# Optimization experiments

Hardware: AMD Instinct MI355X
Metric: run time of the kernel (lower is better)

## Reference

```python
import jax, jax.numpy as jnp
import numpy as np

GROUPS = 8
EPS = 1e-3  # keras GroupNormalization default epsilon


def group_norm(x, gamma, beta):
    # x: [B,H,W,C], groups over channel axis
    B, H, W, C = x.shape
    g = GROUPS
    xr = x.reshape(B, H, W, g, C // g)
    mean = jnp.mean(xr, axis=(1, 2, 4), keepdims=True)
    var = jnp.var(xr, axis=(1, 2, 4), keepdims=True)
    xn = (xr - mean) * jax.lax.rsqrt(var + EPS)
    xn = xn.reshape(B, H, W, C)
    return xn * gamma + beta


def setup_inputs() -> dict:
    key = jax.random.key(0)
    ks = jax.random.split(key, 6)
    B, H, W, C = 8, 64, 64, 64
    std = 0.02
    return {
        "x": jax.random.normal(ks[0], (B, H, W, C), dtype=jnp.float32),
        "gamma": jnp.ones((C,), dtype=jnp.float32),
        "beta": jnp.zeros((C,), dtype=jnp.float32),
        "wq": jax.random.normal(ks[1], (C, C), dtype=jnp.float32) * std,
        "bq": jnp.zeros((C,), dtype=jnp.float32),
        "wk": jax.random.normal(ks[2], (C, C), dtype=jnp.float32) * std,
        "bk": jnp.zeros((C,), dtype=jnp.float32),
        "wv": jax.random.normal(ks[3], (C, C), dtype=jnp.float32) * std,
        "bv": jnp.zeros((C,), dtype=jnp.float32),
        "wp": jax.random.normal(ks[4], (C, C), dtype=jnp.float32) * std,
        "bp": jnp.zeros((C,), dtype=jnp.float32),
    }


def reference(x, gamma, beta, wq, bq, wk, bk, wv, bv, wp, bp):
    B, H, W, C = x.shape
    scale = jnp.asarray(C, x.dtype) ** -0.5
    h = group_norm(x, gamma, beta)  # note: residual uses normalized input (as in source)
    q = h @ wq + bq
    k = h @ wk + bk
    v = h @ wv + bv
    # full O((HW)^2) score tensor, exactly as the original
    attn = jnp.einsum('bhwc,bHWc->bhwHW', q, k) * scale
    attn = jax.nn.softmax(attn.reshape(B, H, W, H * W), axis=-1)
    attn = attn.reshape(B, H, W, H, W)
    proj = jnp.einsum('bhwHW,bHWc->bhwc', attn, v)
    proj = proj @ wp + bp
    return h + proj
```

## Files before the change

### kernel.cpp

```cpp
#include <hip/hip_runtime.h>

#define NTOK 4096
#define CH 64
#define LOG2E 1.4426950408889634f

typedef __bf16 bf8 __attribute__((ext_vector_type(8)));
typedef __bf16 bf4 __attribute__((ext_vector_type(4)));
typedef _Float16 h8 __attribute__((ext_vector_type(8)));
typedef _Float16 h4 __attribute__((ext_vector_type(4)));
typedef float f4 __attribute__((ext_vector_type(4)));

__device__ __forceinline__ f4 mfma16(bf8 a, bf8 b, f4 c) {
    return __builtin_amdgcn_mfma_f32_16x16x32_bf16(a, b, c, 0, 0, 0);
}
__device__ __forceinline__ f4 mfma16h(h4 a, h4 b, f4 c) {
    return __builtin_amdgcn_mfma_f32_16x16x16f16(a, b, c, 0, 0, 0);
}

__global__ __launch_bounds__(256) void pre_kernel(const float* __restrict__ wq,
                                                  const float* __restrict__ wk,
                                                  const float* __restrict__ wv,
                                                  const float* __restrict__ wp,
                                                  const float* __restrict__ x,
                                                  __bf16* __restrict__ wqt,
                                                  __bf16* __restrict__ wkt,
                                                  __bf16* __restrict__ wvt,
                                                  __bf16* __restrict__ wpt,
                                                  float* __restrict__ gpart) {
    int t = threadIdx.x;
    if (blockIdx.x < 4) {
        int m = blockIdx.x;
        const float* src = (m == 0) ? wq : (m == 1) ? wk : (m == 2) ? wv : wp;
        __bf16* dst      = (m == 0) ? wqt : (m == 1) ? wkt : (m == 2) ? wvt : wpt;
        __shared__ float s[64][65];
        for (int i = 0; i < 16; ++i) {
            int e = i * 256 + t;
            s[e >> 6][e & 63] = src[e];
        }
        __syncthreads();
        int out = t >> 2, seg = t & 3;
        for (int j = 0; j < 16; ++j) {
            int in = seg * 16 + j;
            dst[out * 64 + in] = (__bf16)s[in][out];
        }
        return;
    }
    int bid = blockIdx.x - 4;
    int b = bid >> 6, slab = bid & 63;
    const float4* xb = (const float4*)(x + (size_t)(b * NTOK + slab * 64) * CH);
    float s = 0.f, ss = 0.f;
    for (int i = 0; i < 4; ++i) {
        int row = (t >> 4) + i * 16;
        float4 v = xb[row * 16 + (t & 15)];
        s  += v.x + v.y + v.z + v.w;
        ss += v.x * v.x + v.y * v.y + v.z * v.z + v.w * v.w;
    }
    __shared__ float ls[256], lss[256];
    ls[t] = s; lss[t] = ss;
    __syncthreads();
    if (t < 8) {
        float a = 0.f, aa = 0.f;
        for (int p = 0; p < 16; ++p) {
            a  += ls[p * 16 + 2 * t]  + ls[p * 16 + 2 * t + 1];
            aa += lss[p * 16 + 2 * t] + lss[p * 16 + 2 * t + 1];
        }
        gpart[((b * 64 + slab) * 8 + t) * 2 + 0] = a;
        gpart[((b * 64 + slab) * 8 + t) * 2 + 1] = aa;
    }
}

__global__ __launch_bounds__(256) void qkv_gn(const float* __restrict__ x,
                                              const float* __restrict__ gpart,
                                              const float* __restrict__ gamma,
                                              const float* __restrict__ beta,
                                              const __bf16* __restrict__ wqt,
                                              const __bf16* __restrict__ wkt,
                                              const __bf16* __restrict__ wvt,
                                              const float* __restrict__ bq,
                                              const float* __restrict__ bk,
                                              const float* __restrict__ bv,
                                              __bf16* __restrict__ q,
                                              __bf16* __restrict__ k,
                                              _Float16* __restrict__ vT) {
    __shared__ __bf16 W[3][64][72];
    __shared__ __bf16 Hl[64][72];
    __shared__ _Float16 Vst[64][68];
    __shared__ float red[128];
    __shared__ float sstat[16];
    int t = threadIdx.x;
    size_t rowbase = (size_t)blockIdx.x * 64;
    int b = (int)(rowbase >> 12), tokbase = (int)(rowbase & 4095);
    if (t < 64) {
        int gi = t & 7, c = t >> 3;
        const float2* gp = (const float2*)gpart + (size_t)b * 64 * 8 + gi;
        float a = 0.f, aa = 0.f;
        for (int p = c * 8; p < c * 8 + 8; ++p) {
            float2 v = gp[(size_t)p * 8];
            a += v.x; aa += v.y;
        }
        red[t * 2] = a; red[t * 2 + 1] = aa;
    }
    for (int m = 0; m < 3; ++m) {
        const __bf16* src = (m == 0) ? wqt : (m == 1) ? wkt : wvt;
        for (int i = 0; i < 2; ++i) {
            int e = i * 256 + t, row = e >> 3, ch = e & 7;
            *(bf8*)&W[m][row][ch * 8] = *(const bf8*)(src + row * 64 + ch * 8);
        }
    }
    __syncthreads();
    if (t < 8) {
        float a = 0.f, aa = 0.f;
        for (int c = 0; c < 8; ++c) {
            a  += red[(c * 8 + t) * 2];
            aa += red[(c * 8 + t) * 2 + 1];
        }
        float mean = a * (1.f / 32768.f);
        float var = aa * (1.f / 32768.f) - mean * mean;
        sstat[t * 2 + 0] = mean;
        sstat[t * 2 + 1] = rsqrtf(var + 1e-3f);
    }
    __syncthreads();
    {
        int c4 = (t & 15) * 4, grp = c4 >> 3;
        float mean = sstat[grp * 2], rstd = sstat[grp * 2 + 1];
        float g0 = gamma[c4] * rstd, g1 = gamma[c4 + 1] * rstd,
              g2 = gamma[c4 + 2] * rstd, g3 = gamma[c4 + 3] * rstd;
        float b0 = beta[c4], b1 = beta[c4 + 1], b2 = beta[c4 + 2], b3 = beta[c4 + 3];
        const float4* xb = (const float4*)(x + rowbase * 64);
        for (int i = 0; i < 4; ++i) {
            int row = (t >> 4) + i * 16;
            float4 v = xb[row * 16 + (t & 15)];
            bf4 hv;
            hv[0] = (__bf16)((v.x - mean) * g0 + b0);
            hv[1] = (__bf16)((v.y - mean) * g1 + b1);
            hv[2] = (__bf16)((v.z - mean) * g2 + b2);
            hv[3] = (__bf16)((v.w - mean) * g3 + b3);
            *(bf4*)&Hl[row][c4] = hv;
        }
    }
    __syncthreads();
    int lane = t & 63, wave = t >> 6, quad = lane >> 4, l15 = lane & 15;
    bf8 a0 = *(const bf8*)&Hl[wave * 16 + l15][quad * 8];
    bf8 a1 = *(const bf8*)&Hl[wave * 16 + l15][32 + quad * 8];
    for (int m = 0; m < 3; ++m) {
        const float* bias = (m == 0) ? bq : (m == 1) ? bk : bv;
        float sc = (m == 0) ? 0.125f * LOG2E : 1.0f;
        for (int tt = 0; tt < 4; ++tt) {
            int col = l15 + 16 * tt;
            bf8 b0 = *(const bf8*)&W[m][col][quad * 8];
            bf8 b1 = *(const bf8*)&W[m][col][32 + quad * 8];
            f4 acc = {0.f, 0.f, 0.f, 0.f};
            acc = mfma16(a0, b0, acc);
            acc = mfma16(a1, b1, acc);
            float bb = bias[col];
            if (m == 2) {
                for (int r = 0; r < 4; ++r)
                    Vst[col][wave * 16 + quad * 4 + r] = (_Float16)(acc[r] + bb);
            } else {
                __bf16* dst = (m == 0) ? q : k;
                for (int r = 0; r < 4; ++r) {
                    float val = (acc[r] + bb) * sc;
                    dst[(rowbase + wave * 16 + quad * 4 + r) * 64 + col] = (__bf16)val;
                }
            }
        }
    }
    __syncthreads();
    {
        int d = t >> 2, seg = t & 3;
        h4 c0 = *(const h4*)&Vst[d][seg * 16 + 0];
        h4 c1 = *(const h4*)&Vst[d][seg * 16 + 4];
        h4 c2 = *(const h4*)&Vst[d][seg * 16 + 8];
        h4 c3 = *(const h4*)&Vst[d][seg * 16 + 12];
        h8 o0 = {c0[0], c0[1], c0[2], c0[3], c1[0], c1[1], c1[2], c1[3]};
        h8 o1 = {c2[0], c2[1], c2[2], c2[3], c3[0], c3[1], c3[2], c3[3]};
        _Float16* dst = vT + (((size_t)b * 256 + (tokbase >> 4) + seg) * 64 + d) * 16;
        *(h8*)dst = o0;
        *(h8*)(dst + 8) = o1;
    }
}

__global__ __launch_bounds__(256, 2) void attn_final(const __bf16* __restrict__ q,
                                                     const __bf16* __restrict__ k,
                                                     const _Float16* __restrict__ vt,
                                                     const __bf16* __restrict__ wpt,
                                                     const float* __restrict__ bp,
                                                     const float* __restrict__ x,
                                                     const float* __restrict__ gpart,
                                                     const float* __restrict__ gamma,
                                                     const float* __restrict__ beta,
                                                     float* __restrict__ out) {
    __shared__ _Float16 Om[2][64][72];
    __shared__ float sS[2][64];
    __shared__ __bf16 Wl[64][72];
    __shared__ __bf16 Ol[64][72];
    __shared__ float red[128];
    __shared__ float sstat[16], sg[64], sb[64];

    int bid = blockIdx.x;
    int qt = bid >> 3, b = bid & 7;
    int t = threadIdx.x, lane = t & 63, w = t >> 6, quad = lane >> 4, l15 = lane & 15;

    for (int i = 0; i < 2; ++i) {
        int e = i * 256 + t, row = e >> 3, ch = e & 7;
        *(bf8*)&Wl[row][ch * 8] = *(const bf8*)(wpt + row * 64 + ch * 8);
    }
    if (t < 64) { sg[t] = gamma[t]; sb[t] = beta[t]; }
    if (t < 64) {
        int gi = t & 7, c = t >> 3;
        const float2* gp = (const float2*)gpart + (size_t)b * 512 + gi;
        float a = 0.f, aa = 0.f;
        for (int p = c * 8; p < c * 8 + 8; ++p) {
            float2 v = gp[(size_t)p * 8];
            a += v.x; aa += v.y;
        }
        red[t * 2] = a; red[t * 2 + 1] = aa;
    }

    const __bf16* qbase = q + ((size_t)b * NTOK + qt * 64) * 64;
    bf8 aq[4][2];
    for (int s = 0; s < 4; ++s) {
        const __bf16* r = qbase + (s * 16 + l15) * 64;
        aq[s][0] = *(const bf8*)(r + quad * 8);
        aq[s][1] = *(const bf8*)(r + 32 + quad * 8);
    }
    const __bf16* kr = k + ((size_t)b * NTOK + w * 1024 + l15) * 64;
    const _Float16* vr = vt + (size_t)b * 262144 + ((size_t)(w * 64) * 64 + l15) * 16 + quad * 4;

    f4 acc[4][4] = {};
    float li[4] = {0.f, 0.f, 0.f, 0.f};

    bf8 kf0 = *(const bf8*)(kr + quad * 8);
    bf8 kf1 = *(const bf8*)(kr + 32 + quad * 8);
    h4 vf0 = *(const h4*)(vr);
    h4 vf1 = *(const h4*)(vr + 256);
    h4 vf2 = *(const h4*)(vr + 512);
    h4 vf3 = *(const h4*)(vr + 768);

    #pragma unroll 1
    for (int it = 0; it < 64; ++it) {
        int nx = (it + 1) & 63;
        const __bf16* krn = kr + (size_t)nx * 1024;
        const _Float16* vrn = vr + (size_t)nx * 1024;
        bf8 nk0 = *(const bf8*)(krn + quad * 8);
        bf8 nk1 = *(const bf8*)(krn + 32 + quad * 8);
        h4 nv0 = *(const h4*)(vrn);
        h4 nv1 = *(const h4*)(vrn + 256);
        h4 nv2 = *(const h4*)(vrn + 512);
        h4 nv3 = *(const h4*)(vrn + 768);

        for (int s = 0; s < 4; ++s) {
            f4 St = {0.f, 0.f, 0.f, 0.f};
            St = mfma16(kf0, aq[s][0], St);
            St = mfma16(kf1, aq[s][1], St);
            h4 pf;
            for (int r = 0; r < 4; ++r) {
                float pv = __builtin_amdgcn_exp2f(St[r]);
                li[s] += pv;
                pf[r] = (_Float16)pv;
            }
            acc[s][0] = mfma16h(vf0, pf, acc[s][0]);
            acc[s][1] = mfma16h(vf1, pf, acc[s][1]);
            acc[s][2] = mfma16h(vf2, pf, acc[s][2]);
            acc[s][3] = mfma16h(vf3, pf, acc[s][3]);
        }
        kf0 = nk0; kf1 = nk1;
        vf0 = nv0; vf1 = nv1; vf2 = nv2; vf3 = nv3;
    }

    for (int s = 0; s < 4; ++s) {
        li[s] += __shfl_xor(li[s], 16);
        li[s] += __shfl_xor(li[s], 32);
    }

    if (w >= 2) {
        for (int s = 0; s < 4; ++s) {
            for (int td = 0; td < 4; ++td) {
                h4 o4;
                for (int r = 0; r < 4; ++r) o4[r] = (_Float16)acc[s][td][r];
                *(h4*)&Om[w - 2][s * 16 + l15][td * 16 + quad * 4] = o4;
            }
            if (quad == 0) sS[w - 2][s * 16 + l15] = li[s];
        }
    }
    __syncthreads();
    if (t < 8) {
        float a = 0.f, aa = 0.f;
        for (int c = 0; c < 8; ++c) {
            a  += red[(c * 8 + t) * 2];
            aa += red[(c * 8 + t) * 2 + 1];
        }
        float mean = a * (1.f / 32768.f);
        float var = aa * (1.f / 32768.f) - mean * mean;
        sstat[t * 2 + 0] = mean;
        sstat[t * 2 + 1] = rsqrtf(var + 1e-3f);
    }
    if (w < 2) {
        for (int s = 0; s < 4; ++s) {
            for (int td = 0; td < 4; ++td) {
                h4 o4 = *(const h4*)&Om[w][s * 16 + l15][td * 16 + quad * 4];
                for (int r = 0; r < 4; ++r) acc[s][td][r] += (float)o4[r];
            }
            li[s] += sS[w][s * 16 + l15];
        }
    }
    __syncthreads();
    if (w < 2) {
        for (int s = 0; s < 4; ++s) {
            for (int td = 0; td < 4; ++td) {
                h4 o4;
                for (int r = 0; r < 4; ++r) o4[r] = (_Float16)acc[s][td][r];
                *(h4*)&Om[w][s * 16 + l15][td * 16 + quad * 4] = o4;
            }
            if (quad == 0) sS[w][s * 16 + l15] = li[s];
        }
    }
    __syncthreads();
    {
        int qq = t >> 2, ds = (t & 3) * 16;
        float inv = 1.f / (sS[0][qq] + sS[1][qq]);
        h8 a0 = *(const h8*)&Om[0][qq][ds];
        h8 b0 = *(const h8*)&Om[0][qq][ds + 8];
        h8 a1 = *(const h8*)&Om[1][qq][ds];
        h8 b1 = *(const h8*)&Om[1][qq][ds + 8];
        bf8 olo, ohi;
        for (int j = 0; j < 8; ++j) {
            olo[j] = (__bf16)(((float)a0[j] + (float)a1[j]) * inv);
            ohi[j] = (__bf16)(((float)b0[j] + (float)b1[j]) * inv);
        }
        *(bf8*)&Ol[qq][ds] = olo;
        *(bf8*)&Ol[qq][ds + 8] = ohi;
    }
    __syncthreads();
    size_t rowbase = ((size_t)b * NTOK + qt * 64) + w * 16;
    bf8 a0 = *(const bf8*)&Ol[w * 16 + l15][quad * 8];
    bf8 a1 = *(const bf8*)&Ol[w * 16 + l15][32 + quad * 8];
    for (int tt = 0; tt < 4; ++tt) {
        int col = l15 + 16 * tt;
        bf8 b0 = *(const bf8*)&Wl[col][quad * 8];
        bf8 b1 = *(const bf8*)&Wl[col][32 + quad * 8];
        f4 pacc = {0.f, 0.f, 0.f, 0.f};
        pacc = mfma16(a0, b0, pacc);
        pacc = mfma16(a1, b1, pacc);
        int grp = col >> 3;
        float mean = sstat[grp * 2], gs = sg[col] * sstat[grp * 2 + 1], bs = sb[col];
        float bias = bp[col];
        for (int r = 0; r < 4; ++r) {
            size_t gi = (rowbase + quad * 4 + r) * 64 + col;
            float h = (x[gi] - mean) * gs + bs;
            out[gi] = pacc[r] + bias + h;
        }
    }
}

extern "C" void kernel_launch(void* const* d_in, const int* in_sizes, int n_in,
                              void* d_out, int out_size, void* d_ws, size_t ws_size,
                              hipStream_t stream) {
    const float* x     = (const float*)d_in[0];
    const float* gamma = (const float*)d_in[1];
    const float* beta  = (const float*)d_in[2];
    const float* wq    = (const float*)d_in[3];
    const float* bq    = (const float*)d_in[4];
    const float* wk    = (const float*)d_in[5];
    const float* bk    = (const float*)d_in[6];
    const float* wv    = (const float*)d_in[7];
    const float* bv    = (const float*)d_in[8];
    const float* wp    = (const float*)d_in[9];
    const float* bp    = (const float*)d_in[10];
    float* out = (float*)d_out;

    char* ws = (char*)d_ws;
    const size_t MB = 1024 * 1024;
    __bf16*   qb   = (__bf16*)(ws);
    __bf16*   kb   = (__bf16*)(ws + 4 * MB);
    _Float16* vtb  = (_Float16*)(ws + 8 * MB);
    __bf16*   wqt  = (__bf16*)(ws + 12 * MB);
    __bf16*   wkt  = (__bf16*)(ws + 12 * MB + 8192);
    __bf16*   wvt  = (__bf16*)(ws + 12 * MB + 16384);
    __bf16*   wpt  = (__bf16*)(ws + 12 * MB + 24576);
    float*    gpart = (float*)(ws + 12 * MB + 32768);

    pre_kernel<<<516, 256, 0, stream>>>(wq, wk, wv, wp, x, wqt, wkt, wvt, wpt, gpart);
    qkv_gn<<<512, 256, 0, stream>>>(x, gpart, gamma, beta, wqt, wkt, wvt, bq, bk, bv, qb, kb, vtb);
    attn_final<<<512, 256, 0, stream>>>(qb, kb, vtb, wpt, bp, x, gpart, gamma, beta, out);
}
```

Measured before the change: 141.0 us.

## Fuse three kernels into one cooperative kernel with grid-wide syncs

Merges the stats/weight-transpose, GN+QKV projection, and attention+output stages into a single cooperative launch of 512 blocks separated by grid.sync() calls, with a shared-memory union reused across phases. The aim is to remove two kernel launch gaps and their tail effects. In exchange it depends on all 512 blocks being co-resident and on grid sync cost, and it falls back to the three launches if the cooperative launch fails. The attention phase also no longer overlaps with other blocks' work across stages.

```diff
diff --git a/kernel.cpp b/kernel.cpp
--- a/kernel.cpp
+++ b/kernel.cpp
@@ -1,4 +1,7 @@
 #include <hip/hip_runtime.h>
+#include <hip/hip_cooperative_groups.h>
+
+namespace cg = cooperative_groups;
 
 #define NTOK 4096
 #define CH 64
@@ -15,6 +18,338 @@
 }
 __device__ __forceinline__ f4 mfma16h(h4 a, h4 b, f4 c) {
     return __builtin_amdgcn_mfma_f32_16x16x16f16(a, b, c, 0, 0, 0);
+}
+
+__global__ __launch_bounds__(256) void fused_all(const float* __restrict__ x,
+                                                 const float* __restrict__ gamma,
+                                                 const float* __restrict__ beta,
+                                                 const float* __restrict__ wq,
+                                                 const float* __restrict__ bq,
+                                                 const float* __restrict__ wk,
+                                                 const float* __restrict__ bk,
+                                                 const float* __restrict__ wv,
+                                                 const float* __restrict__ bv,
+                                                 const float* __restrict__ wp,
+                                                 const float* __restrict__ bp,
+                                                 __bf16* __restrict__ q,
+                                                 __bf16* __restrict__ k,
+                                                 _Float16* __restrict__ vT,
+                                                 __bf16* __restrict__ wqt,
+                                                 __bf16* __restrict__ wkt,
+                                                 __bf16* __restrict__ wvt,
+                                                 __bf16* __restrict__ wpt,
+                                                 float* __restrict__ gpart,
+                                                 float* __restrict__ out) {
+    __shared__ __align__(16) char smem[46144];
+    int t = threadIdx.x;
+    int bid = blockIdx.x;
+
+    {
+        float* ls  = (float*)(smem + 16640);
+        float* lss = (float*)(smem + 17664);
+        int b = bid >> 6, slab = bid & 63;
+        const float4* xb = (const float4*)(x + (size_t)(b * NTOK + slab * 64) * CH);
+        float s = 0.f, ss = 0.f;
+        for (int i = 0; i < 4; ++i) {
+            int row = (t >> 4) + i * 16;
+            float4 v = xb[row * 16 + (t & 15)];
+            s  += v.x + v.y + v.z + v.w;
+            ss += v.x * v.x + v.y * v.y + v.z * v.z + v.w * v.w;
+        }
+        ls[t] = s; lss[t] = ss;
+        __syncthreads();
+        if (t < 8) {
+            float a = 0.f, aa = 0.f;
+            for (int p = 0; p < 16; ++p) {
+                a  += ls[p * 16 + 2 * t]  + ls[p * 16 + 2 * t + 1];
+                aa += lss[p * 16 + 2 * t] + lss[p * 16 + 2 * t + 1];
+            }
+            gpart[((b * 64 + slab) * 8 + t) * 2 + 0] = a;
+            gpart[((b * 64 + slab) * 8 + t) * 2 + 1] = aa;
+        }
+        if (bid < 4) {
+            float (*ts)[65] = (float (*)[65])(smem);
+            const float* src = (bid == 0) ? wq : (bid == 1) ? wk : (bid == 2) ? wv : wp;
+            __bf16* dst      = (bid == 0) ? wqt : (bid == 1) ? wkt : (bid == 2) ? wvt : wpt;
+            for (int i = 0; i < 16; ++i) {
+                int e = i * 256 + t;
+                ts[e >> 6][e & 63] = src[e];
+            }
+            __syncthreads();
+            int o = t >> 2, seg = t & 3;
+            for (int j = 0; j < 16; ++j) {
+                int in = seg * 16 + j;
+                dst[o * 64 + in] = (__bf16)ts[in][o];
+            }
+        }
+    }
+
+    cg::this_grid().sync();
+
+    {
+        __bf16 (*W)[64][72] = (__bf16 (*)[64][72])(smem);
+        __bf16 (*Hl)[72]    = (__bf16 (*)[72])(smem + 27648);
+        _Float16 (*Vst)[68] = (_Float16 (*)[68])(smem + 36864);
+        float* red   = (float*)(smem + 45568);
+        float* sstat = (float*)(smem + 46080);
+        size_t rowbase = (size_t)bid * 64;
+        int b = (int)(rowbase >> 12), tokbase = (int)(rowbase & 4095);
+        if (t < 64) {
+            int gi = t & 7, c = t >> 3;
+            const float2* gp = (const float2*)gpart + (size_t)b * 512 + gi;
+            float a = 0.f, aa = 0.f;
+            for (int p = c * 8; p < c * 8 + 8; ++p) {
+                float2 v = gp[(size_t)p * 8];
+                a += v.x; aa += v.y;
+            }
+            red[t * 2] = a; red[t * 2 + 1] = aa;
+        }
+        for (int m = 0; m < 3; ++m) {
+            const __bf16* src = (m == 0) ? wqt : (m == 1) ? wkt : wvt;
+            for (int i = 0; i < 2; ++i) {
+                int e = i * 256 + t, row = e >> 3, ch = e & 7;
+                *(bf8*)&W[m][row][ch * 8] = *(const bf8*)(src + row * 64 + ch * 8);
+            }
+        }
+        __syncthreads();
+        if (t < 8) {
+            float a = 0.f, aa = 0.f;
+            for (int c = 0; c < 8; ++c) {
+                a  += red[(c * 8 + t) * 2];
+                aa += red[(c * 8 + t) * 2 + 1];
+            }
+            float mean = a * (1.f / 32768.f);
+            float var = aa * (1.f / 32768.f) - mean * mean;
+            sstat[t * 2 + 0] = mean;
+            sstat[t * 2 + 1] = rsqrtf(var + 1e-3f);
+        }
+        __syncthreads();
+        {
+            int c4 = (t & 15) * 4, grp = c4 >> 3;
+            float mean = sstat[grp * 2], rstd = sstat[grp * 2 + 1];
+            float g0 = gamma[c4] * rstd, g1 = gamma[c4 + 1] * rstd,
+                  g2 = gamma[c4 + 2] * rstd, g3 = gamma[c4 + 3] * rstd;
+            float b0 = beta[c4], b1 = beta[c4 + 1], b2 = beta[c4 + 2], b3 = beta[c4 + 3];
+            const float4* xb = (const float4*)(x + rowbase * 64);
+            for (int i = 0; i < 4; ++i) {
+                int row = (t >> 4) + i * 16;
+                float4 v = xb[row * 16 + (t & 15)];
+                bf4 hv;
+                hv[0] = (__bf16)((v.x - mean) * g0 + b0);
+                hv[1] = (__bf16)((v.y - mean) * g1 + b1);
+                hv[2] = (__bf16)((v.z - mean) * g2 + b2);
+                hv[3] = (__bf16)((v.w - mean) * g3 + b3);
+                *(bf4*)&Hl[row][c4] = hv;
+            }
+        }
+        __syncthreads();
+        int lane = t & 63, wave = t >> 6, quad = lane >> 4, l15 = lane & 15;
+        bf8 a0 = *(const bf8*)&Hl[wave * 16 + l15][quad * 8];
+        bf8 a1 = *(const bf8*)&Hl[wave * 16 + l15][32 + quad * 8];
+        for (int m = 0; m < 3; ++m) {
+            const float* bias = (m == 0) ? bq : (m == 1) ? bk : bv;
+            float sc = (m == 0) ? 0.125f * LOG2E : 1.0f;
+            for (int tt = 0; tt < 4; ++tt) {
+                int col = l15 + 16 * tt;
+                bf8 b0 = *(const bf8*)&W[m][col][quad * 8];
+                bf8 b1 = *(const bf8*)&W[m][col][32 + quad * 8];
+                f4 acc = {0.f, 0.f, 0.f, 0.f};
+                acc = mfma16(a0, b0, acc);
+                acc = mfma16(a1, b1, acc);
+                float bb = bias[col];
+                if (m == 2) {
+                    for (int r = 0; r < 4; ++r)
+                        Vst[col][wave * 16 + quad * 4 + r] = (_Float16)(acc[r] + bb);
+                } else {
+                    __bf16* dst = (m == 0) ? q : k;
+                    for (int r = 0; r < 4; ++r) {
+                        float val = (acc[r] + bb) * sc;
+                        dst[(rowbase + wave * 16 + quad * 4 + r) * 64 + col] = (__bf16)val;
+                    }
+                }
+            }
+        }
+        __syncthreads();
+        {
+            int d = t >> 2, seg = t & 3;
+            h4 c0 = *(const h4*)&Vst[d][seg * 16 + 0];
+            h4 c1 = *(const h4*)&Vst[d][seg * 16 + 4];
+            h4 c2 = *(const h4*)&Vst[d][seg * 16 + 8];
+            h4 c3 = *(const h4*)&Vst[d][seg * 16 + 12];
+            h8 o0 = {c0[0], c0[1], c0[2], c0[3], c1[0], c1[1], c1[2], c1[3]};
+            h8 o1 = {c2[0], c2[1], c2[2], c2[3], c3[0], c3[1], c3[2], c3[3]};
+            _Float16* dst = vT + (((size_t)b * 256 + (tokbase >> 4) + seg) * 64 + d) * 16;
+            *(h8*)dst = o0;
+            *(h8*)(dst + 8) = o1;
+        }
+    }
+
+    cg::this_grid().sync();
+
+    {
+        _Float16 (*Om)[64][72] = (_Float16 (*)[64][72])(smem);
+        float (*sS)[64] = (float (*)[64])(smem + 18432);
+        __bf16 (*Wl)[72] = (__bf16 (*)[72])(smem + 18944);
+        __bf16 (*Ol)[72] = (__bf16 (*)[72])(smem + 28160);
+        float* red   = (float*)(smem + 37376);
+        float* sstat = (float*)(smem + 37888);
+        float* sg    = (float*)(smem + 37952);
+        float* sb    = (float*)(smem + 38208);
+
+        int qt = bid >> 3, b = bid & 7;
+        int lane = t & 63, w = t >> 6, quad = lane >> 4, l15 = lane & 15;
+
+        for (int i = 0; i < 2; ++i) {
+            int e = i * 256 + t, row = e >> 3, ch = e & 7;
+            *(bf8*)&Wl[row][ch * 8] = *(const bf8*)(wpt + row * 64 + ch * 8);
+        }
+        if (t < 64) { sg[t] = gamma[t]; sb[t] = beta[t]; }
+        if (t < 64) {
+            int gi = t & 7, c = t >> 3;
+            const float2* gp = (const float2*)gpart + (size_t)b * 512 + gi;
+            float a = 0.f, aa = 0.f;
+            for (int p = c * 8; p < c * 8 + 8; ++p) {
+                float2 v = gp[(size_t)p * 8];
+                a += v.x; aa += v.y;
+            }
+            red[t * 2] = a; red[t * 2 + 1] = aa;
+        }
+
+        const __bf16* qbase = q + ((size_t)b * NTOK + qt * 64) * 64;
+        bf8 aq[4][2];
+        for (int s = 0; s < 4; ++s) {
+            const __bf16* r = qbase + (s * 16 + l15) * 64;
+            aq[s][0] = *(const bf8*)(r + quad * 8);
+            aq[s][1] = *(const bf8*)(r + 32 + quad * 8);
+        }
+        const __bf16* kr = k + ((size_t)b * NTOK + w * 1024 + l15) * 64;
+        const _Float16* vr = vT + (size_t)b * 262144 + ((size_t)(w * 64) * 64 + l15) * 16 + quad * 4;
+
+        f4 acc[4][4] = {};
+        float li[4] = {0.f, 0.f, 0.f, 0.f};
+
+        bf8 kf0 = *(const bf8*)(kr + quad * 8);
+        bf8 kf1 = *(const bf8*)(kr + 32 + quad * 8);
+        h4 vf0 = *(const h4*)(vr);
+        h4 vf1 = *(const h4*)(vr + 256);
+        h4 vf2 = *(const h4*)(vr + 512);
+        h4 vf3 = *(const h4*)(vr + 768);
+
+        #pragma unroll 1
+        for (int it = 0; it < 64; ++it) {
+            int nx = (it + 1) & 63;
+            const __bf16* krn = kr + (size_t)nx * 1024;
+            const _Float16* vrn = vr + (size_t)nx * 1024;
+            bf8 nk0 = *(const bf8*)(krn + quad * 8);
+            bf8 nk1 = *(const bf8*)(krn + 32 + quad * 8);
+            h4 nv0 = *(const h4*)(vrn);
+            h4 nv1 = *(const h4*)(vrn + 256);
+            h4 nv2 = *(const h4*)(vrn + 512);
+            h4 nv3 = *(const h4*)(vrn + 768);
+
+            for (int s = 0; s < 4; ++s) {
+                f4 St = {0.f, 0.f, 0.f, 0.f};
+                St = mfma16(kf0, aq[s][0], St);
+                St = mfma16(kf1, aq[s][1], St);
+                h4 pf;
+                for (int r = 0; r < 4; ++r) {
+                    float pv = __builtin_amdgcn_exp2f(St[r]);
+                    li[s] += pv;
+                    pf[r] = (_Float16)pv;
+                }
+                acc[s][0] = mfma16h(vf0, pf, acc[s][0]);
+                acc[s][1] = mfma16h(vf1, pf, acc[s][1]);
+                acc[s][2] = mfma16h(vf2, pf, acc[s][2]);
+                acc[s][3] = mfma16h(vf3, pf, acc[s][3]);
+            }
+            kf0 = nk0; kf1 = nk1;
+            vf0 = nv0; vf1 = nv1; vf2 = nv2; vf3 = nv3;
+        }
+
+        for (int s = 0; s < 4; ++s) {
+            li[s] += __shfl_xor(li[s], 16);
+            li[s] += __shfl_xor(li[s], 32);
+        }
+
+        if (w >= 2) {
+            for (int s = 0; s < 4; ++s) {
+                for (int td = 0; td < 4; ++td) {
+                    h4 o4;
+                    for (int r = 0; r < 4; ++r) o4[r] = (_Float16)acc[s][td][r];
+                    *(h4*)&Om[w - 2][s * 16 + l15][td * 16 + quad * 4] = o4;
+                }
+                if (quad == 0) sS[w - 2][s * 16 + l15] = li[s];
+            }
+        }
+        __syncthreads();
+        if (t < 8) {
+            float a = 0.f, aa = 0.f;
+            for (int c = 0; c < 8; ++c) {
+                a  += red[(c * 8 + t) * 2];
+                aa += red[(c * 8 + t) * 2 + 1];
+            }
+            float mean = a * (1.f / 32768.f);
+            float var = aa * (1.f / 32768.f) - mean * mean;
+            sstat[t * 2 + 0] = mean;
+            sstat[t * 2 + 1] = rsqrtf(var + 1e-3f);
+        }
+        if (w < 2) {
+            for (int s = 0; s < 4; ++s) {
+                for (int td = 0; td < 4; ++td) {
+                    h4 o4 = *(const h4*)&Om[w][s * 16 + l15][td * 16 + quad * 4];
+                    for (int r = 0; r < 4; ++r) acc[s][td][r] += (float)o4[r];
+                }
+                li[s] += sS[w][s * 16 + l15];
+            }
+        }
+        __syncthreads();
+        if (w < 2) {
+            for (int s = 0; s < 4; ++s) {
+                for (int td = 0; td < 4; ++td) {
+                    h4 o4;
+                    for (int r = 0; r < 4; ++r) o4[r] = (_Float16)acc[s][td][r];
+                    *(h4*)&Om[w][s * 16 + l15][td * 16 + quad * 4] = o4;
+                }
+                if (quad == 0) sS[w][s * 16 + l15] = li[s];
+            }
+        }
+        __syncthreads();
+        {
+            int qq = t >> 2, ds = (t & 3) * 16;
+            float inv = 1.f / (sS[0][qq] + sS[1][qq]);
+            h8 a0 = *(const h8*)&Om[0][qq][ds];
+            h8 b0 = *(const h8*)&Om[0][qq][ds + 8];
+            h8 a1 = *(const h8*)&Om[1][qq][ds];
+            h8 b1 = *(const h8*)&Om[1][qq][ds + 8];
+            bf8 olo, ohi;
+            for (int j = 0; j < 8; ++j) {
+                olo[j] = (__bf16)(((float)a0[j] + (float)a1[j]) * inv);
+                ohi[j] = (__bf16)(((float)b0[j] + (float)b1[j]) * inv);
+            }
+            *(bf8*)&Ol[qq][ds] = olo;
+            *(bf8*)&Ol[qq][ds + 8] = ohi;
+        }
+        __syncthreads();
+        size_t rowbase = ((size_t)b * NTOK + qt * 64) + w * 16;
+        bf8 a0 = *(const bf8*)&Ol[w * 16 + l15][quad * 8];
+        bf8 a1 = *(const bf8*)&Ol[w * 16 + l15][32 + quad * 8];
+        for (int tt = 0; tt < 4; ++tt) {
+            int col = l15 + 16 * tt;
+            bf8 b0 = *(const bf8*)&Wl[col][quad * 8];
+            bf8 b1 = *(const bf8*)&Wl[col][32 + quad * 8];
+            f4 pacc = {0.f, 0.f, 0.f, 0.f};
+            pacc = mfma16(a0, b0, pacc);
+            pacc = mfma16(a1, b1, pacc);
+            int grp = col >> 3;
+            float mean = sstat[grp * 2], gs = sg[col] * sstat[grp * 2 + 1], bs = sb[col];
+            float bias = bp[col];
+            for (int r = 0; r < 4; ++r) {
+                size_t gi = (rowbase + quad * 4 + r) * 64 + col;
+                float h = (x[gi] - mean) * gs + bs;
+                out[gi] = pacc[r] + bias + h;
+            }
+        }
+    }
 }
 
 __global__ __launch_bounds__(256) void pre_kernel(const float* __restrict__ wq,
@@ -38,10 +373,10 @@
             s[e >> 6][e & 63] = src[e];
         }
         __syncthreads();
-        int out = t >> 2, seg = t & 3;
+        int o = t >> 2, seg = t & 3;
         for (int j = 0; j < 16; ++j) {
             int in = seg * 16 + j;
-            dst[out * 64 + in] = (__bf16)s[in][out];
+            dst[o * 64 + in] = (__bf16)s[in][o];
         }
         return;
     }
@@ -92,7 +427,7 @@
     int b = (int)(rowbase >> 12), tokbase = (int)(rowbase & 4095);
     if (t < 64) {
         int gi = t & 7, c = t >> 3;
-        const float2* gp = (const float2*)gpart + (size_t)b * 64 * 8 + gi;
+        const float2* gp = (const float2*)gpart + (size_t)b * 512 + gi;
         float a = 0.f, aa = 0.f;
         for (int p = c * 8; p < c * 8 + 8; ++p) {
             float2 v = gp[(size_t)p * 8];
@@ -380,7 +715,18 @@
     __bf16*   wpt  = (__bf16*)(ws + 12 * MB + 24576);
     float*    gpart = (float*)(ws + 12 * MB + 32768);
 
-    pre_kernel<<<516, 256, 0, stream>>>(wq, wk, wv, wp, x, wqt, wkt, wvt, wpt, gpart);
-    qkv_gn<<<512, 256, 0, stream>>>(x, gpart, gamma, beta, wqt, wkt, wvt, bq, bk, bv, qb, kb, vtb);
-    attn_final<<<512, 256, 0, stream>>>(qb, kb, vtb, wpt, bp, x, gpart, gamma, beta, out);
+    void* args[] = {(void*)&x, (void*)&gamma, (void*)&beta,
+                    (void*)&wq, (void*)&bq, (void*)&wk, (void*)&bk,
+                    (void*)&wv, (void*)&bv, (void*)&wp, (void*)&bp,
+                    (void*)&qb, (void*)&kb, (void*)&vtb,
+                    (void*)&wqt, (void*)&wkt, (void*)&wvt, (void*)&wpt,
+                    (void*)&gpart, (void*)&out};
+    hipError_t err = hipLaunchCooperativeKernel((void*)fused_all, dim3(512), dim3(256),
+                                                args, 0, stream);
+    if (err != hipSuccess) {
+        pre_kernel<<<516, 256, 0, stream>>>(wq, wk, wv, wp, x, wqt, wkt, wvt, wpt, gpart);
+        qkv_gn<<<512, 256, 0, stream>>>(x, gpart, gamma, beta, wqt, wkt, wvt,
+                                        bq, bk, bv, qb, kb, vtb);
+        attn_final<<<512, 256, 0, stream>>>(qb, kb, vtb, wpt, bp, x, gpart, gamma, beta, out);
+    }
 }
```

Result: slower. 293.0 us (+107.9%).
